# Kernel tuning notes

Hardware: AMD Instinct MI355X
Metric: run time of the kernel (lower is better)

The kernel has to match this reference:

```python
import jax, jax.numpy as jnp
import numpy as np

HEADS = 4
HID = 610
KER = 50  # cov2KerSize
NEG_SLOPE = 0.2


def gat_layer(x, src, dst, w, b, att_src, att_dst, n_nodes):
    # x: [N, Fin], w: [HEADS*HID, Fin], att_*: [1, HEADS, HID], b: [HID]
    h = (x @ w.T).reshape(n_nodes, HEADS, HID)               # [N,H,D]
    a_src = (h * att_src).sum(-1)                            # [N,H]
    a_dst = (h * att_dst).sum(-1)                            # [N,H]
    alpha = jax.nn.leaky_relu(a_src[src] + a_dst[dst], NEG_SLOPE)  # [E,H]
    # softmax over edges grouped by destination node
    m = jax.ops.segment_max(alpha, dst, num_segments=n_nodes)
    e = jnp.exp(alpha - m[dst])
    denom = jax.ops.segment_sum(e, dst, num_segments=n_nodes)
    a = e / (denom[dst] + 1e-16)                             # [E,H]
    msg = h[src] * a[:, :, None]                             # [E,H,D]
    out = jax.ops.segment_sum(msg, dst, num_segments=n_nodes)  # [N,H,D]
    return out.mean(axis=1) + b                              # [N,D] (concat=False)


def setup_inputs() -> dict:
    key = jax.random.key(0)
    ks = jax.random.split(key, 16)
    N, E, FIN, NOUT = 20000, 100000, 128, 86
    x = jax.random.normal(ks[0], (N, FIN), dtype=jnp.float32)
    edge_index = jax.random.randint(ks[1], (2, E), 0, N, dtype=jnp.int64)
    def kaiming(k, shape, fan_in):
        return jax.random.normal(k, shape, dtype=jnp.float32) * np.float32(np.sqrt(2.0 / fan_in))
    w0 = kaiming(ks[2], (HEADS * HID, FIN), FIN)
    b0 = jnp.zeros((HID,), jnp.float32)
    att_src0 = kaiming(ks[3], (1, HEADS, HID), HID)
    att_dst0 = kaiming(ks[4], (1, HEADS, HID), HID)
    w2 = kaiming(ks[5], (HEADS * HID, HID), HID)
    b2 = jnp.zeros((HID,), jnp.float32)
    att_src1 = kaiming(ks[6], (1, HEADS, HID), HID)
    att_dst1 = kaiming(ks[7], (1, HEADS, HID), HID)
    w4 = kaiming(ks[8], (1, 1, 2, KER), 2 * KER)
    b4 = jnp.zeros((1,), jnp.float32)
    w6 = kaiming(ks[9], (1, 1, KER), KER)
    b6 = jnp.zeros((1,), jnp.float32)
    w8 = kaiming(ks[10], (NOUT, 512), 512)
    b8 = jnp.zeros((NOUT,), jnp.float32)
    return dict(x=x, edge_index=edge_index, w0=w0, b0=b0, att_src0=att_src0,
                att_dst0=att_dst0, w2=w2, b2=b2, att_src1=att_src1,
                att_dst1=att_dst1, w4=w4, b4=b4, w6=w6, b6=b6, w8=w8, b8=b8)


def reference(x, edge_index, w0, b0, att_src0, att_dst0, w2, b2, att_src1,
              att_dst1, w4, b4, w6, b6, w8, b8):
    N = x.shape[0]
    src, dst = edge_index[0], edge_index[1]
    x1 = jax.nn.relu(gat_layer(x, src, dst, w0, b0, att_src0, att_dst0, N))
    x2 = jax.nn.relu(gat_layer(x1, src, dst, w2, b2, att_src1, att_dst1, N))
    # edge features: cat(src_feat, dst_feat) viewed as [E,1,2,HID]
    ef = jnp.stack([x2[src], x2[dst]], axis=1)[:, None, :, :]  # [E,1,2,HID]
    y = jax.lax.conv_general_dilated(ef, w4, (1, 1), 'VALID',
                                     dimension_numbers=('NCHW', 'OIHW', 'NCHW'))
    y = jax.nn.relu(y + b4[None, :, None, None])               # [E,1,1,561]
    y = y.reshape(-1, HID - KER + 1, 1).transpose(0, 2, 1)     # [E,1,561]
    y = jax.lax.conv_general_dilated(y, w6, (1,), 'VALID',
                                     dimension_numbers=('NCH', 'OIH', 'NCH'))
    y = jax.nn.relu(y + b6[None, :, None])                     # [E,1,512]
    # adaptive_avg_pool1d to 512 is identity since length is already 512
    y = y.reshape(-1, 512)
    return y @ w8.T + b8                                       # [E, num_outputs]
```

## Files before the change

### kernel.cpp

```cpp
#include <hip/hip_runtime.h>
#include <math.h>

#define HEADS 4
#define HID 610
#define HIDP 640
#define FIN 128
#define KER 50
#define NOUT 86
#define NEG_SLOPE 0.2f

#define Y1S 616
#define ZSS 520

typedef short bf8_t __attribute__((ext_vector_type(8)));
typedef float f4_t __attribute__((ext_vector_type(4)));

__device__ __forceinline__ ushort f2bf(float f) {
    unsigned u = __float_as_uint(f);
    unsigned r = (u + 0x7FFFu + ((u >> 16) & 1u)) >> 16;
    return (ushort)r;
}
__device__ __forceinline__ ushort f2bf_t(float f) {
    return (ushort)(__float_as_uint(f) >> 16);
}
__device__ __forceinline__ float bf2f(ushort b) { return __uint_as_float(((unsigned)b) << 16); }

__global__ void fill_val(float* __restrict__ p, float v, long n) {
    long i = (long)blockIdx.x * blockDim.x + threadIdx.x;
    if (i < n) p[i] = v;
}

__global__ void copy_int(const int* __restrict__ a, int* __restrict__ b, int n) {
    int i = blockIdx.x * blockDim.x + threadIdx.x;
    if (i < n) b[i] = a[i];
}

__global__ void hist_k(const int* __restrict__ ei, int* __restrict__ hist, int E) {
    int e = blockIdx.x * blockDim.x + threadIdx.x;
    if (e < E) atomicAdd(&hist[ei[E + e]], 1);
}

__global__ __launch_bounds__(1024) void scan_k(const int* __restrict__ hist,
                                               int* __restrict__ base, int Nn) {
    __shared__ int tmp[1024];
    __shared__ int carry;
    if (threadIdx.x == 0) carry = 0;
    __syncthreads();
    for (int c0 = 0; c0 < Nn; c0 += 1024) {
        int i = c0 + threadIdx.x;
        int v = (i < Nn) ? hist[i] : 0;
        tmp[threadIdx.x] = v;
        __syncthreads();
        for (int off = 1; off < 1024; off <<= 1) {
            int t = (threadIdx.x >= off) ? tmp[threadIdx.x - off] : 0;
            __syncthreads();
            tmp[threadIdx.x] += t;
            __syncthreads();
        }
        if (i < Nn) base[i] = carry + tmp[threadIdx.x] - v;
        __syncthreads();
        if (threadIdx.x == 1023) carry += tmp[1023];
        __syncthreads();
    }
    if (threadIdx.x == 0) base[Nn] = carry;
}

__global__ void scatter_k(const int* __restrict__ ei, int* __restrict__ cursor,
                          int* __restrict__ esrc, int E) {
    int e = blockIdx.x * blockDim.x + threadIdx.x;
    if (e >= E) return;
    int d = ei[E + e];
    int pos = atomicAdd(&cursor[d], 1);
    esrc[pos] = ei[e];
}

__global__ void split_pad(const float* __restrict__ in, ushort* __restrict__ hi,
                          ushort* __restrict__ lo, int R, int K, int Kp) {
    long i = (long)blockIdx.x * blockDim.x + threadIdx.x;
    if (i >= (long)R * Kp) return;
    int r = (int)(i / Kp), c = (int)(i % Kp);
    float v = (c < K) ? in[(long)r * K + c] : 0.f;
    ushort h = f2bf(v);
    hi[i] = h;
    lo[i] = f2bf(v - bf2f(h));
}

__global__ void build_toeplitz(const float* __restrict__ w4, const float* __restrict__ w6,
                               ushort* __restrict__ T) {
    int i = blockIdx.x * blockDim.x + threadIdx.x;
    if (i >= 18 * 512) return;
    int e = i & 7;
    int lane = (i >> 3) & 63;
    int f = i >> 9;
    int n = lane & 15;
    int k = ((lane >> 4) << 3) + e;
    float wv;
    int hilo;
    if (f < 12) {
        int c = f % 3, hc = f / 3;
        int ch = hc & 1;
        hilo = hc >> 1;
        int d = c * 32 + k - n;
        wv = (d >= 0 && d < KER) ? w4[ch * KER + d] : 0.f;
    } else {
        int r2 = f - 12;
        int c = r2 % 3;
        hilo = r2 / 3;
        int d = c * 32 + k - n;
        wv = (d >= 0 && d < KER) ? w6[d] : 0.f;
    }
    ushort h = f2bf(wv);
    T[i] = hilo ? f2bf(wv - bf2f(h)) : h;
}

template <int AMODE, bool BIAS>
__global__ __launch_bounds__(256) void gemm_mfma(const float* __restrict__ A,
                                                 const ushort* __restrict__ Aghi,
                                                 const ushort* __restrict__ Aglo,
                                                 const ushort* __restrict__ Bghi,
                                                 const ushort* __restrict__ Bglo,
                                                 const float* __restrict__ bias,
                                                 float* __restrict__ C,
                                                 int M, int N, int Kp) {
    __shared__ __align__(16) ushort Ah[128 * 32];
    __shared__ __align__(16) ushort Al[128 * 32];
    __shared__ __align__(16) ushort Bh[128 * 32];
    __shared__ __align__(16) ushort Bl[128 * 32];
    int tid = threadIdx.x;
    int wave = tid >> 6, lane = tid & 63;
    int quad = lane >> 4, l16 = lane & 15;
    int wm = wave & 1, wn = wave >> 1;
    int row0 = blockIdx.y * 128, col0 = blockIdx.x * 128;

    float4 pa0[4];
    uint4 pah[2], pal[2], pbh[2], pbl[2];

    auto loadA = [&](int k0) {
        if (AMODE == 0) {
#pragma unroll
            for (int q = 0; q < 4; q++) {
                int p = tid + q * 256;
                int r = p >> 3, c4 = (p & 7) << 2;
                int gr = row0 + r;
                pa0[q] = (gr < M) ? *(const float4*)(A + (size_t)gr * Kp + k0 + c4)
                                  : make_float4(0.f, 0.f, 0.f, 0.f);
            }
        } else {
#pragma unroll
            for (int q = 0; q < 2; q++) {
                int p = tid + q * 256;
                int r = p >> 2, c = p & 3;
                int gr = row0 + r;
                if (gr < M) {
                    pah[q] = *(const uint4*)(Aghi + (size_t)gr * Kp + k0 + c * 8);
                    pal[q] = *(const uint4*)(Aglo + (size_t)gr * Kp + k0 + c * 8);
                } else {
                    pah[q] = make_uint4(0, 0, 0, 0);
                    pal[q] = make_uint4(0, 0, 0, 0);
                }
            }
        }
    };
    auto loadB = [&](int k0) {
#pragma unroll
        for (int q = 0; q < 2; q++) {
            int p = tid + q * 256;
            int r = p >> 2, c = p & 3;
            int gr = col0 + r;
            if (gr < N) {
                pbh[q] = *(const uint4*)(Bghi + (size_t)gr * Kp + k0 + c * 8);
                pbl[q] = *(const uint4*)(Bglo + (size_t)gr * Kp + k0 + c * 8);
            } else {
                pbh[q] = make_uint4(0, 0, 0, 0);
                pbl[q] = make_uint4(0, 0, 0, 0);
            }
        }
    };
    auto writeLDS = [&]() {
        if (AMODE == 0) {
#pragma unroll
            for (int q = 0; q < 4; q++) {
                int p = tid + q * 256;
                int r = p >> 3, m = p & 7;
                int pos = r * 32 + ((((m >> 1)) ^ ((r >> 1) & 3)) << 3) + ((m & 1) << 2);
                float4 v = pa0[q];
                ushort4 hv, lv;
                hv.x = f2bf(v.x); lv.x = f2bf(v.x - bf2f(hv.x));
                hv.y = f2bf(v.y); lv.y = f2bf(v.y - bf2f(hv.y));
                hv.z = f2bf(v.z); lv.z = f2bf(v.z - bf2f(hv.z));
                hv.w = f2bf(v.w); lv.w = f2bf(v.w - bf2f(hv.w));
                *(ushort4*)&Ah[pos] = hv;
                *(ushort4*)&Al[pos] = lv;
            }
        } else {
#pragma unroll
            for (int q = 0; q < 2; q++) {
                int p = tid + q * 256;
                int r = p >> 2, c = p & 3;
                int pos = r * 32 + ((c ^ ((r >> 1) & 3)) << 3);
                *(uint4*)&Ah[pos] = pah[q];
                *(uint4*)&Al[pos] = pal[q];
            }
        }
#pragma unroll
        for (int q = 0; q < 2; q++) {
            int p = tid + q * 256;
            int r = p >> 2, c = p & 3;
            int pos = r * 32 + ((c ^ ((r >> 1) & 3)) << 3);
            *(uint4*)&Bh[pos] = pbh[q];
            *(uint4*)&Bl[pos] = pbl[q];
        }
    };

    f4_t acc[4][4];
#pragma unroll
    for (int i = 0; i < 4; i++)
#pragma unroll
        for (int j = 0; j < 4; j++) acc[i][j] = (f4_t){0.f, 0.f, 0.f, 0.f};

    loadA(0);
    loadB(0);
    int sw = (quad ^ ((l16 >> 1) & 3)) << 3;
    for (int k0 = 0; k0 < Kp; k0 += 32) {
        __syncthreads();
        writeLDS();
        __syncthreads();
        if (k0 + 32 < Kp) {
            loadA(k0 + 32);
            loadB(k0 + 32);
        }
        bf8_t ah[4], al[4], bh[4], bl[4];
#pragma unroll
        for (int t = 0; t < 4; t++) {
            int ar = wm * 64 + t * 16 + l16;
            ah[t] = *(const bf8_t*)&Ah[ar * 32 + sw];
            al[t] = *(const bf8_t*)&Al[ar * 32 + sw];
            int br = wn * 64 + t * 16 + l16;
            bh[t] = *(const bf8_t*)&Bh[br * 32 + sw];
            bl[t] = *(const bf8_t*)&Bl[br * 32 + sw];
        }
#pragma unroll
        for (int i = 0; i < 4; i++)
#pragma unroll
            for (int j = 0; j < 4; j++) {
                acc[i][j] = __builtin_amdgcn_mfma_f32_16x16x32_bf16(ah[i], bh[j], acc[i][j], 0, 0, 0);
                acc[i][j] = __builtin_amdgcn_mfma_f32_16x16x32_bf16(al[i], bh[j], acc[i][j], 0, 0, 0);
                acc[i][j] = __builtin_amdgcn_mfma_f32_16x16x32_bf16(ah[i], bl[j], acc[i][j], 0, 0, 0);
            }
    }
#pragma unroll
    for (int i = 0; i < 4; i++) {
#pragma unroll
        for (int r = 0; r < 4; r++) {
            int grow = row0 + wm * 64 + i * 16 + quad * 4 + r;
            if (grow >= M) continue;
#pragma unroll
            for (int j = 0; j < 4; j++) {
                int gcol = col0 + wn * 64 + j * 16 + l16;
                if (gcol >= N) continue;
                float v = acc[i][j][r];
                if (BIAS) v += bias[gcol];
                C[(size_t)grow * N + gcol] = v;
            }
        }
    }
}

__global__ __launch_bounds__(256) void attn_dots(const float* __restrict__ h,
                                                 const float* __restrict__ att_s,
                                                 const float* __restrict__ att_d,
                                                 float* __restrict__ a_src,
                                                 float* __restrict__ a_dst, int Nn) {
    int n = blockIdx.x;
    int head = threadIdx.x >> 6;
    int lane = threadIdx.x & 63;
    const float2* hr = (const float2*)(h + (long)n * (HEADS * HID) + head * HID);
    const float2* as = (const float2*)(att_s + head * HID);
    const float2* ad = (const float2*)(att_d + head * HID);
    float ss = 0.f, sd = 0.f;
    for (int d = lane; d < HID / 2; d += 64) {
        float2 hv = hr[d], av = as[d], dv = ad[d];
        ss += hv.x * av.x + hv.y * av.y;
        sd += hv.x * dv.x + hv.y * dv.y;
    }
    for (int off = 32; off > 0; off >>= 1) {
        ss += __shfl_down(ss, off);
        sd += __shfl_down(sd, off);
    }
    if (lane == 0) {
        a_src[n * HEADS + head] = ss;
        a_dst[n * HEADS + head] = sd;
    }
}

template <int OUTMODE>
__global__ __launch_bounds__(256) void node_aggregate(
    const float* __restrict__ h, const float* __restrict__ asrc,
    const float* __restrict__ adst, const int* __restrict__ base,
    const int* __restrict__ esrc, const float* __restrict__ bias,
    float* __restrict__ xout, ushort* __restrict__ xhi, ushort* __restrict__ xlo,
    int Nn) {
    int wave = threadIdx.x >> 6, lane = threadIdx.x & 63;
    int n = blockIdx.x * 4 + wave;
    if (n >= Nn) return;
    int b0 = base[n], deg = base[n + 1] - b0;
    float ad[HEADS];
#pragma unroll
    for (int hh = 0; hh < HEADS; hh++) ad[hh] = adst[n * HEADS + hh];
    float m[HEADS] = {-INFINITY, -INFINITY, -INFINITY, -INFINITY};
    for (int eb = 0; eb < deg; eb += 64) {
        int i = eb + lane;
        if (i < deg) {
            int s = esrc[b0 + i];
#pragma unroll
            for (int hh = 0; hh < HEADS; hh++) {
                float v = asrc[s * HEADS + hh] + ad[hh];
                v = v >= 0.f ? v : NEG_SLOPE * v;
                m[hh] = fmaxf(m[hh], v);
            }
        }
    }
#pragma unroll
    for (int off = 32; off > 0; off >>= 1)
#pragma unroll
        for (int hh = 0; hh < HEADS; hh++) m[hh] = fmaxf(m[hh], __shfl_xor(m[hh], off));
    float sden[HEADS] = {0.f, 0.f, 0.f, 0.f};
    for (int eb = 0; eb < deg; eb += 64) {
        int i = eb + lane;
        if (i < deg) {
            int s = esrc[b0 + i];
#pragma unroll
            for (int hh = 0; hh < HEADS; hh++) {
                float v = asrc[s * HEADS + hh] + ad[hh];
                v = v >= 0.f ? v : NEG_SLOPE * v;
                sden[hh] += expf(v - m[hh]);
            }
        }
    }
#pragma unroll
    for (int off = 32; off > 0; off >>= 1)
#pragma unroll
        for (int hh = 0; hh < HEADS; hh++) sden[hh] += __shfl_xor(sden[hh], off);
    float inv[HEADS];
#pragma unroll
    for (int hh = 0; hh < HEADS; hh++) inv[hh] = 0.25f / (sden[hh] + 1e-16f);
    float acc0[10] = {}, acc1[10] = {}, acc2[10] = {}, acc3[10] = {};
    for (int eb = 0; eb < deg; eb += 64) {
        int i = eb + lane;
        int sreg = 0;
        float coef[HEADS] = {0.f, 0.f, 0.f, 0.f};
        if (i < deg) {
            sreg = esrc[b0 + i];
#pragma unroll
            for (int hh = 0; hh < HEADS; hh++) {
                float v = asrc[sreg * HEADS + hh] + ad[hh];
                v = v >= 0.f ? v : NEG_SLOPE * v;
                coef[hh] = expf(v - m[hh]) * inv[hh];
            }
        }
        int cnt = deg - eb < 64 ? deg - eb : 64;
        for (int j = 0; j < cnt; j++) {
            int s = __shfl(sreg, j);
            float c0 = __shfl(coef[0], j), c1 = __shfl(coef[1], j);
            float c2 = __shfl(coef[2], j), c3 = __shfl(coef[3], j);
            const float* hr = h + (size_t)s * (HEADS * HID);
#pragma unroll
            for (int t = 0; t < 10; t++) {
                int d = lane + t * 64;
                if (d < HID) {
                    acc0[t] = fmaf(c0, hr[d], acc0[t]);
                    acc1[t] = fmaf(c1, hr[HID + d], acc1[t]);
                    acc2[t] = fmaf(c2, hr[2 * HID + d], acc2[t]);
                    acc3[t] = fmaf(c3, hr[3 * HID + d], acc3[t]);
                }
            }
        }
    }
#pragma unroll
    for (int t = 0; t < 10; t++) {
        int d = lane + t * 64;
        if (d < HID) {
            float v = acc0[t] + acc1[t] + acc2[t] + acc3[t] + bias[d];
            v = v > 0.f ? v : 0.f;
            if (OUTMODE == 0) {
                xout[(size_t)n * HIDP + d] = v;
            } else {
                ushort hv = f2bf(v);
                xhi[(size_t)n * HIDP + d] = hv;
                xlo[(size_t)n * HIDP + d] = f2bf(v - bf2f(hv));
            }
        }
    }
    for (int d = HID + lane; d < HIDP; d += 64) {
        if (OUTMODE == 0) {
            xout[(size_t)n * HIDP + d] = 0.f;
        } else {
            xhi[(size_t)n * HIDP + d] = 0;
            xlo[(size_t)n * HIDP + d] = 0;
        }
    }
}

__global__ __launch_bounds__(256, 2) void edge_fused(
    const ushort* __restrict__ x2hi, const ushort* __restrict__ x2lo,
    const int* __restrict__ ei, const ushort* __restrict__ T,
    const float* __restrict__ b4, const float* __restrict__ b6,
    const ushort* __restrict__ w8hi, const ushort* __restrict__ w8lo,
    const float* __restrict__ b8, float* __restrict__ out, int E) {
    __shared__ __align__(16) ushort y1h[32 * Y1S];
    __shared__ __align__(16) ushort y1l[32 * Y1S];
    const int tid = threadIdx.x;
    const int wave = tid >> 6, lane = tid & 63;
    const int quad = lane >> 4, l16 = lane & 15;
    const int e0 = blockIdx.x * 32;
    const int et = wave & 1;
    const int p = wave >> 1;
    const int p16 = p * 16;

    int eidx = e0 + et * 16 + l16;
    if (eidx >= E) eidx = E - 1;
    const ushort* psh = x2hi + (size_t)ei[eidx] * HIDP + quad * 8;
    const ushort* psl = x2lo + (size_t)ei[eidx] * HIDP + quad * 8;
    const ushort* pth = x2hi + (size_t)ei[E + eidx] * HIDP + quad * 8;
    const ushort* ptl = x2lo + (size_t)ei[E + eidx] * HIDP + quad * 8;

    bf8_t Wsh[8], Wsl[8], Wth[8], Wtl[8];
#define LDCH(slot, m)                                     \
    {                                                     \
        const int o_ = p16 + 32 * (m);                    \
        Wsh[slot] = *(const bf8_t*)(psh + o_);            \
        Wth[slot] = *(const bf8_t*)(pth + o_);            \
        if ((m) <= 18) {                                  \
            Wsl[slot] = *(const bf8_t*)(psl + o_);        \
            Wtl[slot] = *(const bf8_t*)(ptl + o_);        \
        }                                                 \
    }
#pragma unroll
    for (int m = 0; m < 7; m++) LDCH(m, m);

    for (int i = tid; i < 32 * (Y1S - 576); i += 256) {
        int r = i / (Y1S - 576);
        int j = 576 + (i - r * (Y1S - 576));
        y1h[r * Y1S + j] = 0;
        y1l[r * Y1S + j] = 0;
    }

    bf8_t B1h[2][3], B1l[2][2];
#pragma unroll
    for (int ch = 0; ch < 2; ch++) {
#pragma unroll
        for (int c = 0; c < 3; c++)
            B1h[ch][c] = *(const bf8_t*)&T[(ch * 3 + c) * 512 + lane * 8];
#pragma unroll
        for (int c = 0; c < 2; c++)
            B1l[ch][c] = *(const bf8_t*)&T[((2 + ch) * 3 + c) * 512 + lane * 8];
    }
    const float bb4 = b4[0], bb6 = b6[0];

#pragma unroll
    for (int t = 0; t < 18; t++) {
        if (t <= 12) LDCH((t + 7) & 7, t + 7);
        const int c0 = t & 7, c1 = (t + 1) & 7, c2 = (t + 2) & 7;
        f4_t acc = {bb4, bb4, bb4, bb4};
        acc = __builtin_amdgcn_mfma_f32_16x16x32_bf16(Wsh[c0], B1h[0][0], acc, 0, 0, 0);
        acc = __builtin_amdgcn_mfma_f32_16x16x32_bf16(Wsl[c0], B1h[0][0], acc, 0, 0, 0);
        acc = __builtin_amdgcn_mfma_f32_16x16x32_bf16(Wsh[c0], B1l[0][0], acc, 0, 0, 0);
        acc = __builtin_amdgcn_mfma_f32_16x16x32_bf16(Wth[c0], B1h[1][0], acc, 0, 0, 0);
        acc = __builtin_amdgcn_mfma_f32_16x16x32_bf16(Wtl[c0], B1h[1][0], acc, 0, 0, 0);
        acc = __builtin_amdgcn_mfma_f32_16x16x32_bf16(Wth[c0], B1l[1][0], acc, 0, 0, 0);
        acc = __builtin_amdgcn_mfma_f32_16x16x32_bf16(Wsh[c1], B1h[0][1], acc, 0, 0, 0);
        acc = __builtin_amdgcn_mfma_f32_16x16x32_bf16(Wsl[c1], B1h[0][1], acc, 0, 0, 0);
        acc = __builtin_amdgcn_mfma_f32_16x16x32_bf16(Wsh[c1], B1l[0][1], acc, 0, 0, 0);
        acc = __builtin_amdgcn_mfma_f32_16x16x32_bf16(Wth[c1], B1h[1][1], acc, 0, 0, 0);
        acc = __builtin_amdgcn_mfma_f32_16x16x32_bf16(Wtl[c1], B1h[1][1], acc, 0, 0, 0);
        acc = __builtin_amdgcn_mfma_f32_16x16x32_bf16(Wth[c1], B1l[1][1], acc, 0, 0, 0);
        acc = __builtin_amdgcn_mfma_f32_16x16x32_bf16(Wsh[c2], B1h[0][2], acc, 0, 0, 0);
        acc = __builtin_amdgcn_mfma_f32_16x16x32_bf16(Wth[c2], B1h[1][2], acc, 0, 0, 0);
        const int j0 = p16 + 32 * t;
#pragma unroll
        for (int r = 0; r < 4; r++) {
            int e_ = et * 16 + quad * 4 + r;
            int pos = e_ * Y1S + j0 + l16;
            float v = acc[r];
            v = v > 0.f ? v : 0.f;
            ushort hh = f2bf_t(v);
            y1h[pos] = hh;
            y1l[pos] = f2bf(v - bf2f(hh));
        }
    }
    __syncthreads();

    bf8_t B2h[3], B2l[2];
#pragma unroll
    for (int c = 0; c < 3; c++) B2h[c] = *(const bf8_t*)&T[(12 + c) * 512 + lane * 8];
#pragma unroll
    for (int c = 0; c < 2; c++) B2l[c] = *(const bf8_t*)&T[(15 + c) * 512 + lane * 8];
    const int arow1 = (et * 16 + l16) * Y1S + quad * 8;
    bf8_t Yh[4], Yl[4];
#define LDY(slot, m)                                          \
    {                                                         \
        const int o_ = arow1 + p16 + 32 * (m);                \
        Yh[slot] = *(const bf8_t*)&y1h[o_];                   \
        if ((m) <= 16) Yl[slot] = *(const bf8_t*)&y1l[o_];    \
    }
#pragma unroll
    for (int m = 0; m < 3; m++) LDY(m, m);
    f4_t zac[16];
#pragma unroll
    for (int t = 0; t < 16; t++) {
        if (t <= 14) LDY((t + 3) & 3, t + 3);
        const int c0 = t & 3, c1 = (t + 1) & 3, c2 = (t + 2) & 3;
        f4_t acc = {bb6, bb6, bb6, bb6};
        acc = __builtin_amdgcn_mfma_f32_16x16x32_bf16(Yh[c0], B2h[0], acc, 0, 0, 0);
        acc = __builtin_amdgcn_mfma_f32_16x16x32_bf16(Yl[c0], B2h[0], acc, 0, 0, 0);
        acc = __builtin_amdgcn_mfma_f32_16x16x32_bf16(Yh[c0], B2l[0], acc, 0, 0, 0);
        acc = __builtin_amdgcn_mfma_f32_16x16x32_bf16(Yh[c1], B2h[1], acc, 0, 0, 0);
        acc = __builtin_amdgcn_mfma_f32_16x16x32_bf16(Yl[c1], B2h[1], acc, 0, 0, 0);
        acc = __builtin_amdgcn_mfma_f32_16x16x32_bf16(Yh[c1], B2l[1], acc, 0, 0, 0);
        acc = __builtin_amdgcn_mfma_f32_16x16x32_bf16(Yh[c2], B2h[2], acc, 0, 0, 0);
#pragma unroll
        for (int r = 0; r < 4; r++) {
            float v = acc[r];
            zac[t][r] = v > 0.f ? v : 0.f;
        }
    }
    __syncthreads();

#pragma unroll
    for (int t = 0; t < 16; t++) {
        const int j02 = p16 + 32 * t;
#pragma unroll
        for (int r = 0; r < 4; r++) {
            int e_ = et * 16 + quad * 4 + r;
            int pos = e_ * ZSS + j02 + l16;
            float v = zac[t][r];
            ushort hh = f2bf_t(v);
            y1h[pos] = hh;
            y1l[pos] = f2bf(v - bf2f(hh));
        }
    }
    __syncthreads();

#pragma unroll
    for (int it = 0; it < 3; it++) {
        const int item = wave + it * 4;
        const int et2 = item & 1, nt = item >> 1;
        const int col = nt * 16 + l16;
        const int wrow = col < NOUT ? col : 0;
        const float bias = col < NOUT ? b8[col] : 0.f;
        f4_t acc = {bias, bias, bias, bias};
        const int arow = (et2 * 16 + l16) * ZSS + quad * 8;
        const ushort* wph = w8hi + (size_t)wrow * 512 + quad * 8;
        const ushort* wpl = w8lo + (size_t)wrow * 512 + quad * 8;
#pragma unroll
        for (int c = 0; c < 16; c++) {
            bf8_t zh = *(const bf8_t*)&y1h[arow + c * 32];
            bf8_t zl = *(const bf8_t*)&y1l[arow + c * 32];
            bf8_t wh = *(const bf8_t*)(wph + c * 32);
            bf8_t wl = *(const bf8_t*)(wpl + c * 32);
            acc = __builtin_amdgcn_mfma_f32_16x16x32_bf16(zh, wh, acc, 0, 0, 0);
            acc = __builtin_amdgcn_mfma_f32_16x16x32_bf16(zl, wh, acc, 0, 0, 0);
            acc = __builtin_amdgcn_mfma_f32_16x16x32_bf16(zh, wl, acc, 0, 0, 0);
        }
        if (col < NOUT) {
#pragma unroll
            for (int r = 0; r < 4; r++) {
                int e_ = e0 + et2 * 16 + quad * 4 + r;
                if (e_ < E) out[(size_t)e_ * NOUT + col] = acc[r];
            }
        }
    }
#undef LDCH
#undef LDY
}

extern "C" void kernel_launch(void* const* d_in, const int* in_sizes, int n_in,
                              void* d_out, int out_size, void* d_ws, size_t ws_size,
                              hipStream_t stream) {
    const float* x = (const float*)d_in[0];
    const int* ei = (const int*)d_in[1];
    const float* w0 = (const float*)d_in[2];
    const float* b0 = (const float*)d_in[3];
    const float* att_s0 = (const float*)d_in[4];
    const float* att_d0 = (const float*)d_in[5];
    const float* w2 = (const float*)d_in[6];
    const float* b2 = (const float*)d_in[7];
    const float* att_s1 = (const float*)d_in[8];
    const float* att_d1 = (const float*)d_in[9];
    const float* w4 = (const float*)d_in[10];
    const float* b4 = (const float*)d_in[11];
    const float* w6 = (const float*)d_in[12];
    const float* b6 = (const float*)d_in[13];
    const float* w8 = (const float*)d_in[14];
    const float* b8 = (const float*)d_in[15];
    float* out = (float*)d_out;

    const int Nn = in_sizes[0] / FIN;
    const int E = in_sizes[1] / 2;
    const int HD = HEADS * HID;

    float* ws = (float*)d_ws;
    size_t o = 0;
    float* buf1 = ws + o; o += (size_t)Nn * HIDP;
    ushort* x1hi = (ushort*)buf1;
    ushort* x1lo = x1hi + (size_t)Nn * HIDP;
    ushort* w8hi = (ushort*)(ws + o);
    ushort* w8lo = w8hi + (size_t)NOUT * 512; o += (size_t)NOUT * 512;
    int* base = (int*)(ws + o); o += (size_t)Nn + 4;
    int* cursor = (int*)(ws + o); o += (size_t)Nn;
    int* esrc = (int*)(ws + o); o += (size_t)E;
    float* asrc = ws + o; o += (size_t)Nn * HEADS;
    float* adst = ws + o; o += (size_t)Nn * HEADS;
    ushort* w0hi = (ushort*)(ws + o);
    ushort* w0lo = w0hi + (size_t)HD * FIN; o += (size_t)HD * FIN;
    ushort* w2hi = (ushort*)(ws + o);
    ushort* w2lo = w2hi + (size_t)HD * HIDP; o += (size_t)HD * HIDP;
    float* h = ws + o;

    int edgeGrid = (E + 255) / 256;
    int nodeWaveGrid = (Nn + 3) / 4;
    int fusedGrid = (E + 31) / 32;
    dim3 gGemmL((HD + 127) / 128, (Nn + 127) / 128);

    split_pad<<<((HD * FIN) + 255) / 256, 256, 0, stream>>>(w0, w0hi, w0lo, HD, FIN, FIN);
    split_pad<<<((HD * HIDP) + 255) / 256, 256, 0, stream>>>(w2, w2hi, w2lo, HD, HID, HIDP);
    split_pad<<<((NOUT * 512) + 255) / 256, 256, 0, stream>>>(w8, w8hi, w8lo, NOUT, 512, 512);
    fill_val<<<(Nn + 255) / 256, 256, 0, stream>>>((float*)cursor, 0.f, Nn);
    hist_k<<<edgeGrid, 256, 0, stream>>>(ei, cursor, E);
    scan_k<<<1, 1024, 0, stream>>>(cursor, base, Nn);
    copy_int<<<(Nn + 255) / 256, 256, 0, stream>>>(base, cursor, Nn);
    scatter_k<<<edgeGrid, 256, 0, stream>>>(ei, cursor, esrc, E);

    gemm_mfma<0, false><<<gGemmL, 256, 0, stream>>>(x, nullptr, nullptr, w0hi, w0lo, nullptr,
                                                    h, Nn, HD, FIN);
    build_toeplitz<<<(18 * 512 + 255) / 256, 256, 0, stream>>>(w4, w6, w0hi);
    attn_dots<<<Nn, 256, 0, stream>>>(h, att_s0, att_d0, asrc, adst, Nn);
    node_aggregate<1><<<nodeWaveGrid, 256, 0, stream>>>(h, asrc, adst, base, esrc, b0,
                                                        nullptr, x1hi, x1lo, Nn);

    gemm_mfma<1, false><<<gGemmL, 256, 0, stream>>>(nullptr, x1hi, x1lo, w2hi, w2lo, nullptr,
                                                    h, Nn, HD, HIDP);
    attn_dots<<<Nn, 256, 0, stream>>>(h, att_s1, att_d1, asrc, adst, Nn);
    node_aggregate<1><<<nodeWaveGrid, 256, 0, stream>>>(h, asrc, adst, base, esrc, b2,
                                                        nullptr, x1hi, x1lo, Nn);

    edge_fused<<<fusedGrid, 256, 0, stream>>>(x1hi, x1lo, ei, w0hi, b4, b6,
                                              w8hi, w8lo, b8, out, E);
}
```

Baseline: 1.091 ms.

## Process edges in destination-sorted order with smaller 16-edge blocks in edge kernel

The edge kernel now reads edges in CSR (destination-sorted) order using new edst/eorg arrays written by the scatter pass, so consecutive edges share destination rows for better cache reuse, and output rows are written to their original edge index. The block shrinks from 32 to 16 edges, with waves splitting the conv column range in halves instead of edge tiles. This halves shared memory per block and raises the occupancy target to 4 blocks per SM. The cost is scattered output writes, extra index arrays, and more blocks that each reload Toeplitz and w8 operands.

```diff
diff --git a/kernel.cpp b/kernel.cpp
--- a/kernel.cpp
+++ b/kernel.cpp
@@ -66,12 +66,15 @@
 }
 
 __global__ void scatter_k(const int* __restrict__ ei, int* __restrict__ cursor,
-                          int* __restrict__ esrc, int E) {
+                          int* __restrict__ esrc, int* __restrict__ edst,
+                          int* __restrict__ eorg, int E) {
     int e = blockIdx.x * blockDim.x + threadIdx.x;
     if (e >= E) return;
     int d = ei[E + e];
     int pos = atomicAdd(&cursor[d], 1);
     esrc[pos] = ei[e];
+    edst[pos] = d;
+    eorg[pos] = e;
 }
 
 __global__ void split_pad(const float* __restrict__ in, ushort* __restrict__ hi,
@@ -401,28 +404,30 @@
     }
 }
 
-__global__ __launch_bounds__(256, 2) void edge_fused(
+__global__ __launch_bounds__(256, 4) void edge_fused(
     const ushort* __restrict__ x2hi, const ushort* __restrict__ x2lo,
-    const int* __restrict__ ei, const ushort* __restrict__ T,
+    const int* __restrict__ esrc, const int* __restrict__ edst,
+    const int* __restrict__ eorg, const ushort* __restrict__ T,
     const float* __restrict__ b4, const float* __restrict__ b6,
     const ushort* __restrict__ w8hi, const ushort* __restrict__ w8lo,
     const float* __restrict__ b8, float* __restrict__ out, int E) {
-    __shared__ __align__(16) ushort y1h[32 * Y1S];
-    __shared__ __align__(16) ushort y1l[32 * Y1S];
+    __shared__ __align__(16) ushort y1h[16 * Y1S];
+    __shared__ __align__(16) ushort y1l[16 * Y1S];
     const int tid = threadIdx.x;
     const int wave = tid >> 6, lane = tid & 63;
     const int quad = lane >> 4, l16 = lane & 15;
-    const int e0 = blockIdx.x * 32;
-    const int et = wave & 1;
-    const int p = wave >> 1;
+    const int e0 = blockIdx.x * 16;
+    const int p = wave & 1;
+    const int half = wave >> 1;
     const int p16 = p * 16;
 
-    int eidx = e0 + et * 16 + l16;
-    if (eidx >= E) eidx = E - 1;
-    const ushort* psh = x2hi + (size_t)ei[eidx] * HIDP + quad * 8;
-    const ushort* psl = x2lo + (size_t)ei[eidx] * HIDP + quad * 8;
-    const ushort* pth = x2hi + (size_t)ei[E + eidx] * HIDP + quad * 8;
-    const ushort* ptl = x2lo + (size_t)ei[E + eidx] * HIDP + quad * 8;
+    int i = e0 + l16;
+    if (i >= E) i = E - 1;
+    const int s = esrc[i], d = edst[i];
+    const ushort* psh = x2hi + (size_t)s * HIDP + quad * 8;
+    const ushort* psl = x2lo + (size_t)s * HIDP + quad * 8;
+    const ushort* pth = x2hi + (size_t)d * HIDP + quad * 8;
+    const ushort* ptl = x2lo + (size_t)d * HIDP + quad * 8;
 
     bf8_t Wsh[8], Wsl[8], Wth[8], Wtl[8];
 #define LDCH(slot, m)                                     \
@@ -435,12 +440,13 @@
             Wtl[slot] = *(const bf8_t*)(ptl + o_);        \
         }                                                 \
     }
-#pragma unroll
-    for (int m = 0; m < 7; m++) LDCH(m, m);
-
-    for (int i = tid; i < 32 * (Y1S - 576); i += 256) {
-        int r = i / (Y1S - 576);
-        int j = 576 + (i - r * (Y1S - 576));
+    const int t0 = half * 9;
+#pragma unroll
+    for (int m = 0; m < 7; m++) LDCH((t0 + m) & 7, t0 + m);
+
+    for (int idx = tid; idx < 16 * (Y1S - 576); idx += 256) {
+        int r = idx / (Y1S - 576);
+        int j = 576 + (idx - r * (Y1S - 576));
         y1h[r * Y1S + j] = 0;
         y1l[r * Y1S + j] = 0;
     }
@@ -458,8 +464,9 @@
     const float bb4 = b4[0], bb6 = b6[0];
 
 #pragma unroll
-    for (int t = 0; t < 18; t++) {
-        if (t <= 12) LDCH((t + 7) & 7, t + 7);
+    for (int tt = 0; tt < 9; tt++) {
+        const int t = t0 + tt;
+        if (tt <= 3) LDCH((t + 7) & 7, t + 7);
         const int c0 = t & 7, c1 = (t + 1) & 7, c2 = (t + 2) & 7;
         f4_t acc = {bb4, bb4, bb4, bb4};
         acc = __builtin_amdgcn_mfma_f32_16x16x32_bf16(Wsh[c0], B1h[0][0], acc, 0, 0, 0);
@@ -479,7 +486,7 @@
         const int j0 = p16 + 32 * t;
 #pragma unroll
         for (int r = 0; r < 4; r++) {
-            int e_ = et * 16 + quad * 4 + r;
+            int e_ = quad * 4 + r;
             int pos = e_ * Y1S + j0 + l16;
             float v = acc[r];
             v = v > 0.f ? v : 0.f;
@@ -495,7 +502,7 @@
     for (int c = 0; c < 3; c++) B2h[c] = *(const bf8_t*)&T[(12 + c) * 512 + lane * 8];
 #pragma unroll
     for (int c = 0; c < 2; c++) B2l[c] = *(const bf8_t*)&T[(15 + c) * 512 + lane * 8];
-    const int arow1 = (et * 16 + l16) * Y1S + quad * 8;
+    const int arow1 = l16 * Y1S + quad * 8;
     bf8_t Yh[4], Yl[4];
 #define LDY(slot, m)                                          \
     {                                                         \
@@ -503,12 +510,14 @@
         Yh[slot] = *(const bf8_t*)&y1h[o_];                   \
         if ((m) <= 16) Yl[slot] = *(const bf8_t*)&y1l[o_];    \
     }
-#pragma unroll
-    for (int m = 0; m < 3; m++) LDY(m, m);
-    f4_t zac[16];
-#pragma unroll
-    for (int t = 0; t < 16; t++) {
-        if (t <= 14) LDY((t + 3) & 3, t + 3);
+    const int t0b = half * 8;
+#pragma unroll
+    for (int m = 0; m < 3; m++) LDY((t0b + m) & 3, t0b + m);
+    f4_t zac[8];
+#pragma unroll
+    for (int tt = 0; tt < 8; tt++) {
+        const int t = t0b + tt;
+        if (tt <= 6) LDY((t + 3) & 3, t + 3);
         const int c0 = t & 3, c1 = (t + 1) & 3, c2 = (t + 2) & 3;
         f4_t acc = {bb6, bb6, bb6, bb6};
         acc = __builtin_amdgcn_mfma_f32_16x16x32_bf16(Yh[c0], B2h[0], acc, 0, 0, 0);
@@ -521,19 +530,19 @@
 #pragma unroll
         for (int r = 0; r < 4; r++) {
             float v = acc[r];
-            zac[t][r] = v > 0.f ? v : 0.f;
+            zac[tt][r] = v > 0.f ? v : 0.f;
         }
     }
     __syncthreads();
 
 #pragma unroll
-    for (int t = 0; t < 16; t++) {
-        const int j02 = p16 + 32 * t;
+    for (int tt = 0; tt < 8; tt++) {
+        const int j02 = p16 + 32 * (t0b + tt);
 #pragma unroll
         for (int r = 0; r < 4; r++) {
-            int e_ = et * 16 + quad * 4 + r;
+            int e_ = quad * 4 + r;
             int pos = e_ * ZSS + j02 + l16;
-            float v = zac[t][r];
+            float v = zac[tt][r];
             ushort hh = f2bf_t(v);
             y1h[pos] = hh;
             y1l[pos] = f2bf(v - bf2f(hh));
@@ -542,31 +551,32 @@
     __syncthreads();
 
 #pragma unroll
-    for (int it = 0; it < 3; it++) {
-        const int item = wave + it * 4;
-        const int et2 = item & 1, nt = item >> 1;
-        const int col = nt * 16 + l16;
-        const int wrow = col < NOUT ? col : 0;
-        const float bias = col < NOUT ? b8[col] : 0.f;
-        f4_t acc = {bias, bias, bias, bias};
-        const int arow = (et2 * 16 + l16) * ZSS + quad * 8;
-        const ushort* wph = w8hi + (size_t)wrow * 512 + quad * 8;
-        const ushort* wpl = w8lo + (size_t)wrow * 512 + quad * 8;
-#pragma unroll
-        for (int c = 0; c < 16; c++) {
-            bf8_t zh = *(const bf8_t*)&y1h[arow + c * 32];
-            bf8_t zl = *(const bf8_t*)&y1l[arow + c * 32];
-            bf8_t wh = *(const bf8_t*)(wph + c * 32);
-            bf8_t wl = *(const bf8_t*)(wpl + c * 32);
-            acc = __builtin_amdgcn_mfma_f32_16x16x32_bf16(zh, wh, acc, 0, 0, 0);
-            acc = __builtin_amdgcn_mfma_f32_16x16x32_bf16(zl, wh, acc, 0, 0, 0);
-            acc = __builtin_amdgcn_mfma_f32_16x16x32_bf16(zh, wl, acc, 0, 0, 0);
-        }
-        if (col < NOUT) {
-#pragma unroll
-            for (int r = 0; r < 4; r++) {
-                int e_ = e0 + et2 * 16 + quad * 4 + r;
-                if (e_ < E) out[(size_t)e_ * NOUT + col] = acc[r];
+    for (int it = 0; it < 2; it++) {
+        const int nt = wave + it * 4;
+        if (nt < 6) {
+            const int col = nt * 16 + l16;
+            const int wrow = col < NOUT ? col : 0;
+            const float bias = col < NOUT ? b8[col] : 0.f;
+            f4_t acc = {bias, bias, bias, bias};
+            const int arow = l16 * ZSS + quad * 8;
+            const ushort* wph = w8hi + (size_t)wrow * 512 + quad * 8;
+            const ushort* wpl = w8lo + (size_t)wrow * 512 + quad * 8;
+#pragma unroll
+            for (int c = 0; c < 16; c++) {
+                bf8_t zh = *(const bf8_t*)&y1h[arow + c * 32];
+                bf8_t zl = *(const bf8_t*)&y1l[arow + c * 32];
+                bf8_t wh = *(const bf8_t*)(wph + c * 32);
+                bf8_t wl = *(const bf8_t*)(wpl + c * 32);
+                acc = __builtin_amdgcn_mfma_f32_16x16x32_bf16(zh, wh, acc, 0, 0, 0);
+                acc = __builtin_amdgcn_mfma_f32_16x16x32_bf16(zl, wh, acc, 0, 0, 0);
+                acc = __builtin_amdgcn_mfma_f32_16x16x32_bf16(zh, wl, acc, 0, 0, 0);
+            }
+            if (col < NOUT) {
+#pragma unroll
+                for (int r = 0; r < 4; r++) {
+                    int er = e0 + quad * 4 + r;
+                    if (er < E) out[(size_t)eorg[er] * NOUT + col] = acc[r];
+                }
             }
         }
     }
@@ -609,6 +619,8 @@
     int* base = (int*)(ws + o); o += (size_t)Nn + 4;
     int* cursor = (int*)(ws + o); o += (size_t)Nn;
     int* esrc = (int*)(ws + o); o += (size_t)E;
+    int* edst = (int*)(ws + o); o += (size_t)E;
+    int* eorg = (int*)(ws + o); o += (size_t)E;
     float* asrc = ws + o; o += (size_t)Nn * HEADS;
     float* adst = ws + o; o += (size_t)Nn * HEADS;
     ushort* w0hi = (ushort*)(ws + o);
@@ -619,7 +631,7 @@
 
     int edgeGrid = (E + 255) / 256;
     int nodeWaveGrid = (Nn + 3) / 4;
-    int fusedGrid = (E + 31) / 32;
+    int fusedGrid = (E + 15) / 16;
     dim3 gGemmL((HD + 127) / 128, (Nn + 127) / 128);
 
     split_pad<<<((HD * FIN) + 255) / 256, 256, 0, stream>>>(w0, w0hi, w0lo, HD, FIN, FIN);
@@ -629,7 +641,7 @@
     hist_k<<<edgeGrid, 256, 0, stream>>>(ei, cursor, E);
     scan_k<<<1, 1024, 0, stream>>>(cursor, base, Nn);
     copy_int<<<(Nn + 255) / 256, 256, 0, stream>>>(base, cursor, Nn);
-    scatter_k<<<edgeGrid, 256, 0, stream>>>(ei, cursor, esrc, E);
+    scatter_k<<<edgeGrid, 256, 0, stream>>>(ei, cursor, esrc, edst, eorg, E);
 
     gemm_mfma<0, false><<<gGemmL, 256, 0, stream>>>(x, nullptr, nullptr, w0hi, w0lo, nullptr,
                                                     h, Nn, HD, FIN);
@@ -644,6 +656,6 @@
     node_aggregate<1><<<nodeWaveGrid, 256, 0, stream>>>(h, asrc, adst, base, esrc, b2,
                                                         nullptr, x1hi, x1lo, Nn);
 
-    edge_fused<<<fusedGrid, 256, 0, stream>>>(x1hi, x1lo, ei, w0hi, b4, b6,
+    edge_fused<<<fusedGrid, 256, 0, stream>>>(x1hi, x1lo, esrc, edst, eorg, w0hi, b4, b6,
                                               w8hi, w8lo, b8, out, E);
 }
```

Result: slower. 2.775 ms (+154.5%).
